# Performance work log

Measured on AMD Instinct MI355X. Metric: run time of the kernel, lower is better.

## Reference

```python
import jax, jax.numpy as jnp
import numpy as np
import math

HIDDEN = 768
HEADS = 12
HEAD_DIM = HIDDEN // HEADS
BLOCK = 256
TOPK = 3
BATCH = 2
SEQ = 2048


def setup_inputs() -> dict:
    key = jax.random.key(0)
    ks = jax.random.split(key, 5)
    s = 1.0 / math.sqrt(HIDDEN)
    return {
        "hidden_states": jax.random.normal(ks[0], (BATCH, SEQ, HIDDEN), jnp.float32),
        "Wq": jax.random.normal(ks[1], (HIDDEN, HIDDEN), jnp.float32) * s,
        "Wk": jax.random.normal(ks[2], (HIDDEN, HIDDEN), jnp.float32) * s,
        "Wv": jax.random.normal(ks[3], (HIDDEN, HIDDEN), jnp.float32) * s,
        "Wo": jax.random.normal(ks[4], (HIDDEN, HIDDEN), jnp.float32) * s,
    }


def _rope(x, sin, cos):
    # x: [B, H, S, D]; rotate-half RoPE
    d2 = x.shape[-1] // 2
    x1, x2 = x[..., :d2], x[..., d2:]
    return x * cos + jnp.concatenate([-x2, x1], axis=-1) * sin


def reference(hidden_states, Wq, Wk, Wv, Wo):
    B, S, Hd = hidden_states.shape
    H, D, bs, K = HEADS, HEAD_DIM, BLOCK, TOPK
    nb = S // bs  # number of key blocks
    scale = 1.0 / math.sqrt(D)

    def split_heads(x):
        return x.reshape(B, S, H, D).transpose(0, 2, 1, 3)  # [B,H,S,D]

    q = split_heads(hidden_states @ Wq.T)
    k = split_heads(hidden_states @ Wk.T)
    v = split_heads(hidden_states @ Wv.T)

    # rotary embedding (standard rotate-half RoPE, base 10000)
    inv_freq = 1.0 / (10000.0 ** (jnp.arange(0, D, 2, dtype=jnp.float32) / D))
    ang = jnp.arange(S, dtype=jnp.float32)[:, None] * inv_freq[None, :]  # [S, D/2]
    emb = jnp.concatenate([ang, ang], axis=-1)  # [S, D]
    sin, cos = jnp.sin(emb), jnp.cos(emb)
    q = _rope(q, sin, cos)
    k = _rope(k, sin, cos)

    # mean-pooled block representations of keys: [B,H,nb,D]
    block_reps = k.reshape(B, H, nb, bs, D).mean(axis=3)

    # routing scores: per-token score against each block rep
    bscores = jnp.einsum('bhsd,bhnd->bhsn', q, block_reps) * scale  # [B,H,S,nb]
    pos = jnp.arange(S)
    cur = pos // bs                       # current block of each query, [S]
    blk = jnp.arange(nb)
    future = blk[None, None, None, :] > cur[None, None, :, None]
    bscores = jnp.where(future, -jnp.inf, bscores)
    # current block is force-selected (score set to dtype max)
    is_cur = blk[None, None, None, :] == cur[None, None, :, None]
    bscores = jnp.where(is_cur, jnp.finfo(bscores.dtype).max, bscores)

    _, topk_idx = jax.lax.top_k(bscores, min(K, nb))  # [B,H,S,K]
    selected = jnp.sum(jax.nn.one_hot(topk_idx, nb, dtype=jnp.float32), axis=-2) > 0  # [B,H,S,nb]

    # per-key-position mask: key t allowed iff its block is selected for query i,
    # and within the current block only t <= i (matches original truncation).
    sel_t = selected[:, :, :, cur]                          # [B,H,Sq,Sk]
    intra_ok = (cur[None, :] != cur[:, None]) | (pos[None, :] <= pos[:, None])  # [Sq,Sk]
    mask = sel_t & intra_ok[None, None]

    scores = jnp.einsum('bhqd,bhkd->bhqk', q, k) * scale
    scores = jnp.where(mask, scores, -jnp.inf)
    probs = jax.nn.softmax(scores, axis=-1)
    out = jnp.einsum('bhqk,bhkd->bhqd', probs, v)

    out = out.transpose(0, 2, 1, 3).reshape(B, S, Hd)
    return out @ Wo.T
```

## Files before the change

### kernel.cpp

```cpp
#include <hip/hip_runtime.h>
#include <math.h>


#define HID   768
#define NH    12
#define DH    64
#define SEQN  2048
#define BATCH 2
#define NTOK  (BATCH*SEQN)
#define NB    8
#define BLKSZ 256
#define NEG_INF (-__builtin_huge_valf())
#define POS_INF (__builtin_huge_valf())
#define LO_SCALE 2048.0f
#define LO_INV   (1.0f/2048.0f)
#define EXP2C    0.18033688f

#define SPLIT_ROWS 1024
#define NBH   (BATCH*NH)

typedef unsigned short u16;
typedef _Float16 v8hf __attribute__((ext_vector_type(8)));
typedef float    v4f  __attribute__((ext_vector_type(4)));

__device__ __forceinline__ u16 f2h(float x) {
    _Float16 h = (_Float16)x;
    return __builtin_bit_cast(u16, h);
}
__device__ __forceinline__ float h2f(u16 u) {
    return (float)__builtin_bit_cast(_Float16, u);
}
__device__ __forceinline__ v8hf ldhf8(const u16* p) {
    return *reinterpret_cast<const v8hf*>(p);
}
__device__ __forceinline__ void g2lds16(const u16* g, u16* l) {
    __builtin_amdgcn_global_load_lds(
        (const __attribute__((address_space(1))) void*)g,
        (__attribute__((address_space(3))) void*)l, 16, 0, 0);
}
#define MFMA16(a, b, c) __builtin_amdgcn_mfma_f32_16x16x32_f16(a, b, c, 0, 0, 0)

__global__ __launch_bounds__(256)
void preproc_k(const float* __restrict__ X,  const float* __restrict__ Wq,
               const float* __restrict__ Wk, const float* __restrict__ Wv,
               const float* __restrict__ Wo, float2* __restrict__ tab,
               u16* __restrict__ Xh, u16* __restrict__ Xl,
               u16* __restrict__ Wq2, u16* __restrict__ Wk2,
               u16* __restrict__ Wv2, u16* __restrict__ Wo2)
{
    const int NW = HID * HID;
    const int id = blockIdx.x;
    const int tid = threadIdx.x;
    if (id < 12288) {
        const int i = id * 256 + tid;
        const float x = X[i];
        const u16 h = f2h(x);
        Xh[i] = h;
        Xl[i] = f2h((x - h2f(h)) * LO_SCALE);
    } else if (id < 21504) {
        const int j = (id - 12288) * 256 + tid;
        const int z = j / NW, i = j - z * NW;
        const float* src = (z == 0) ? Wq : (z == 1) ? Wk : (z == 2) ? Wv : Wo;
        u16* dst = (z == 0) ? Wq2 : (z == 1) ? Wk2 : (z == 2) ? Wv2 : Wo2;
        const float x = src[i];
        const u16 h = f2h(x);
        dst[i] = h;
        dst[i + NW] = f2h((x - h2f(h)) * LO_SCALE);
    } else {
        const int i = (id - 21504) * 256 + tid;
        const int s = i >> 5, f = i & 31;
        const double y  = exp((double)f * (log(10000.0) / 32.0));
        const float yf = (float)y;
        const float invf = 1.0f / yf;
        const float ang  = (float)s * invf;
        tab[i] = make_float2((float)sin((double)ang), (float)cos((double)ang));
    }
}

__device__ __forceinline__
void qkv_mainloop(const u16* __restrict__ Ah, const u16* __restrict__ Al,
                  const u16* __restrict__ Bh, const u16* __restrict__ Bl,
                  int m0, int nb0, int c_start,
                  u16* As, u16* Bs, v4f acc[2][4])
{
    const int tid = threadIdx.x;
    const int w = tid >> 6, lane = tid & 63;
    const int col = lane & 15, quad = lane >> 4;

    int a_row[4], a_gl[4];
    #pragma unroll
    for (int r = 0; r < 4; r++) {
        const int g = r * 256 + tid;
        a_row[r] = g >> 3;
        a_gl[r]  = (g & 7) ^ (a_row[r] & 7);
    }
    int b_row[2], b_gl[2];
    #pragma unroll
    for (int r = 0; r < 2; r++) {
        const int g = r * 256 + tid;
        b_row[r] = g >> 3;
        b_gl[r]  = (g & 7) ^ (b_row[r] & 7);
    }

    for (int c = c_start; c < 3; c++) {
        const u16* Ap = (c == 0) ? Al : Ah;
        const u16* Bp = (c == 1) ? Bl : Bh;
        for (int itc = 0; itc < HID / 64; itc++) {
            const int k0 = itc * 64;
            __syncthreads();
            #pragma unroll
            for (int r = 0; r < 4; r++)
                g2lds16(Ap + (size_t)(m0 + a_row[r]) * HID + k0 + a_gl[r] * 8,
                        &As[(r * 256 + w * 64) * 8]);
            #pragma unroll
            for (int r = 0; r < 2; r++)
                g2lds16(Bp + (size_t)(nb0 + b_row[r]) * HID + k0 + b_gl[r] * 8,
                        &Bs[(r * 256 + w * 64) * 8]);
            __syncthreads();
            #pragma unroll
            for (int ks = 0; ks < 2; ks++) {
                v8hf af[2], bf_[4];
                #pragma unroll
                for (int mt = 0; mt < 2; mt++) {
                    const int row = w * 32 + mt * 16 + col;
                    const int gph = (ks * 4 + quad) ^ (row & 7);
                    af[mt] = ldhf8(&As[row * 64 + gph * 8]);
                }
                #pragma unroll
                for (int nt = 0; nt < 4; nt++) {
                    const int row = nt * 16 + col;
                    const int gph = (ks * 4 + quad) ^ (row & 7);
                    bf_[nt] = ldhf8(&Bs[row * 64 + gph * 8]);
                }
                #pragma unroll
                for (int mt = 0; mt < 2; mt++)
                    #pragma unroll
                    for (int nt = 0; nt < 4; nt++)
                        acc[mt][nt] = MFMA16(af[mt], bf_[nt], acc[mt][nt]);
            }
        }
        if (c == 1) {
            #pragma unroll
            for (int mt = 0; mt < 2; mt++)
                #pragma unroll
                for (int nt = 0; nt < 4; nt++)
                    #pragma unroll
                    for (int r = 0; r < 4; r++)
                        acc[mt][nt][r] *= LO_INV;
        }
    }
    __syncthreads();
}

__global__ __launch_bounds__(256)
void qkv_fused_gemm_k(const u16* __restrict__ Xh, const u16* __restrict__ Xl,
                      const u16* __restrict__ Wq2, const u16* __restrict__ Wk2,
                      const u16* __restrict__ Wv2, const float2* __restrict__ tab,
                      float* __restrict__ q32, u16* __restrict__ kh16,
                      u16* __restrict__ vth, float* __restrict__ partial)
{
    __shared__ u16 As[128 * 64];
    __shared__ u16 Bs[64 * 64];
    __shared__ float psum[4][64];

    const int NW = HID * HID;
    const int id    = blockIdx.x;
    const int xcd   = id & 7, loc = id >> 3;
    const int mtile = xcd * 4 + (loc & 3);
    const int ntile = loc >> 2;
    const int m0  = mtile * 128;
    const int mat = ntile / 12;
    const int nb0 = (ntile - mat * 12) * 64;
    const u16* Bh = (mat == 0) ? Wq2 : (mat == 1) ? Wk2 : Wv2;

    v4f acc[2][4] = {};
    qkv_mainloop(Xh, Xl, Bh, Bh + NW, m0, nb0, (mat == 2) ? 1 : 0, As, Bs, acc);

    const int tid = threadIdx.x;
    const int w = tid >> 6, lane = tid & 63;
    const int col = lane & 15, quad = lane >> 4;
    const int b = m0 >> 11;
    const int h = nb0 >> 6;
    const size_t bh = (size_t)b * NH + h;

    if (mat == 2) {
        #pragma unroll
        for (int nt = 0; nt < 4; nt++) {
            const int d = nt * 16 + col;
            #pragma unroll
            for (int mt = 0; mt < 2; mt++) {
                const int m = m0 + w * 32 + mt * 16 + quad * 4;
                const int s = m & (SEQN - 1);
                ushort4 pk = make_ushort4(f2h(acc[mt][nt][0]), f2h(acc[mt][nt][1]),
                                          f2h(acc[mt][nt][2]), f2h(acc[mt][nt][3]));
                *(ushort4*)&vth[(bh * DH + d) * SEQN + s] = pk;
            }
        }
        return;
    }

    float vsum[4] = {0.f, 0.f, 0.f, 0.f};
    #pragma unroll
    for (int mt = 0; mt < 2; mt++) {
        #pragma unroll
        for (int nt = 0; nt < 4; nt++) {
            const int d = nt * 16 + col;
            #pragma unroll
            for (int r = 0; r < 4; r++) {
                const int m = m0 + w * 32 + mt * 16 + quad * 4 + r;
                const int s = m & (SEQN - 1);
                const float part = acc[mt][nt ^ 2][r];
                const float2 sc = tab[(s << 5) + (d & 31)];
                const float val = (d < 32) ? acc[mt][nt][r] * sc.y - part * sc.x
                                           : acc[mt][nt][r] * sc.y + part * sc.x;
                const size_t idx = (bh * SEQN + s) * DH + d;
                if (mat == 0) {
                    q32[idx] = val;
                } else {
                    kh16[idx] = f2h(val);
                    vsum[nt] += val;
                }
            }
        }
    }
    if (mat == 1) {
        #pragma unroll
        for (int nt = 0; nt < 4; nt++) {
            float v = vsum[nt];
            v += __shfl_xor(v, 16);
            v += __shfl_xor(v, 32);
            if (quad == 0) psum[w][nt * 16 + col] = v;
        }
        __syncthreads();
        if (tid < 64) {
            const float s4 = (psum[0][tid] + psum[1][tid])
                           + (psum[2][tid] + psum[3][tid]);
            const int nblk = (m0 & (SEQN - 1)) >> 8;
            const int half = (m0 >> 7) & 1;
            partial[((bh * NB + nblk) * 2 + half) * 64 + tid] = s4;
        }
    }
}

__global__ __launch_bounds__(256)
void out_gemm_mfma_k(const u16* __restrict__ Ah, const u16* __restrict__ Wo2,
                     float* __restrict__ C)
{
    __shared__ u16 As[64 * 64];
    __shared__ u16 Bs[64 * 64];

    const int NW = HID * HID;
    const int id    = blockIdx.x;
    const int xcd   = id & 7, loc = id >> 3;
    const int mtile = xcd * 8 + (loc & 7);
    const int ntile = loc >> 3;
    const int m0 = mtile * 64, n0 = ntile * 64;
    const int tid = threadIdx.x;
    const int w = tid >> 6, lane = tid & 63;
    const int col = lane & 15, quad = lane >> 4;

    const int r0 = tid >> 3,         gl0 = (tid & 7) ^ (r0 & 7);
    const int r1 = (256 + tid) >> 3, gl1 = ((256 + tid) & 7) ^ (r1 & 7);

    v4f acc[4] = {};
    #pragma unroll
    for (int c = 0; c < 2; c++) {
        const u16* Bp = (c == 0) ? (Wo2 + NW) : Wo2;
        for (int itc = 0; itc < HID / 64; itc++) {
            const int k0 = itc * 64;
            __syncthreads();
            g2lds16(Ah + (size_t)(m0 + r0) * HID + k0 + gl0 * 8, &As[(w * 64) * 8]);
            g2lds16(Ah + (size_t)(m0 + r1) * HID + k0 + gl1 * 8, &As[(256 + w * 64) * 8]);
            g2lds16(Bp + (size_t)(n0 + r0) * HID + k0 + gl0 * 8, &Bs[(w * 64) * 8]);
            g2lds16(Bp + (size_t)(n0 + r1) * HID + k0 + gl1 * 8, &Bs[(256 + w * 64) * 8]);
            __syncthreads();
            #pragma unroll
            for (int ks = 0; ks < 2; ks++) {
                const int arow = w * 16 + col;
                v8hf a = ldhf8(&As[arow * 64 + (((ks * 4 + quad) ^ (arow & 7))) * 8]);
                #pragma unroll
                for (int nt = 0; nt < 4; nt++) {
                    const int row = nt * 16 + col;
                    v8hf bb = ldhf8(&Bs[row * 64 + (((ks * 4 + quad) ^ (row & 7))) * 8]);
                    acc[nt] = MFMA16(a, bb, acc[nt]);
                }
            }
        }
        if (c == 0) {
            #pragma unroll
            for (int nt = 0; nt < 4; nt++)
                #pragma unroll
                for (int r = 0; r < 4; r++)
                    acc[nt][r] *= LO_INV;
        }
    }

    #pragma unroll
    for (int nt = 0; nt < 4; nt++)
        #pragma unroll
        for (int r = 0; r < 4; r++) {
            const int m = m0 + w * 16 + quad * 4 + r;
            C[(size_t)m * HID + n0 + nt * 16 + col] = acc[nt][r];
        }
}

__global__ __launch_bounds__(64)
void reps_reduce_k(const float* __restrict__ partial, float* __restrict__ reps)
{
    const int bhn = blockIdx.x;
    const int d = threadIdx.x;
    const float* p = &partial[(size_t)bhn * 128 + d];
    double s = (double)p[0] + (double)p[64];
    reps[(size_t)bhn * 64 + d] = (float)(s * (1.0 / 256.0));
}

__global__ __launch_bounds__(128)
void select_topk_k(const float* __restrict__ qg, const float* __restrict__ reps,
                   unsigned* __restrict__ selm)
{
    __shared__ float rs[NB][DH];
    const int bh = blockIdx.y;
    const int tid = threadIdx.x;
    for (int idx = tid; idx < NB * DH; idx += 128)
        rs[idx >> 6][idx & 63] = reps[(size_t)bh * NB * DH + idx];
    __syncthreads();

    const int qq = blockIdx.x * 128 + tid;
    const float* qv = &qg[((size_t)bh * SEQN + qq) * DH];
    float qr[DH];
    #pragma unroll
    for (int c = 0; c < 16; c++) {
        float4 t = *(const float4*)&qv[c * 4];
        qr[c*4+0]=t.x; qr[c*4+1]=t.y; qr[c*4+2]=t.z; qr[c*4+3]=t.w;
    }
    const int cur = qq >> 8;
    double sc[NB];
    #pragma unroll
    for (int n = 0; n < NB; n++) {
        double ssum = 0.0;
        for (int d = 0; d < DH; d++) ssum += (double)qr[d] * (double)rs[n][d];
        sc[n] = ssum * 0.125;
    }
    for (int n = cur + 1; n < NB; n++) sc[n] = -1e300;
    sc[cur] = 1e300;
    unsigned mask = 0;
    for (int p = 0; p < 3; p++) {
        int bi = -1; double bv = 0.0;
        for (int n = 0; n < NB; n++) {
            if ((mask >> n) & 1) continue;
            if (bi < 0 || sc[n] > bv) { bi = n; bv = sc[n]; }
        }
        mask |= 1u << bi;
    }
    selm[(size_t)bh * SEQN + qq] = mask;
}

__global__ __launch_bounds__(256, 5)
void moba_attn_k(const float* __restrict__ q32, const u16* __restrict__ kh16,
                 const u16* __restrict__ vth, const unsigned* __restrict__ selm,
                 u16* __restrict__ aoh, float* __restrict__ po,
                 float* __restrict__ ml)
{
    __shared__ u16 kbuf[2][64 * 64];
    __shared__ u16 vbuf[64 * 64];
    __shared__ u16 plds[4][16][64];
    unsigned* s_uni = (unsigned*)&plds[0][0][0];

    const int id  = blockIdx.x;
    const int xcd = id & 7, loc = id >> 3;
    const int bh  = xcd * 3 + loc / 48;
    const int u   = loc % 48;
    int qb, split, stride;
    if (u < 16) { qb = u;                 split = 0;          stride = 1; }
    else        { qb = 16 + ((u - 16) >> 1); split = (u - 16) & 1; stride = 2; }
    const int q0  = qb * 64;
    const int cur = q0 >> 8;
    const int tid = threadIdx.x;
    const int wave = tid >> 6, lane = tid & 63;
    const int col = lane & 15, quad = lane >> 4;
    const int qw0 = q0 + wave * 16;
    const int qpos = qw0 + col;
    const size_t bhS = (size_t)bh * SEQN;
    const size_t bhV = (size_t)bh * DH;

    if (tid == 0) *s_uni = 0;
    __syncthreads();
    const unsigned mymask = selm[bhS + qw0 + col];
    unsigned uw = mymask;
    #pragma unroll
    for (int off = 1; off < 16; off <<= 1) uw |= __shfl_xor(uw, off);
    if (lane == 0) atomicOr(s_uni, uw);
    const unsigned wmask = __builtin_amdgcn_readfirstlane(uw);

    v8hf qh[2], ql[2];
    #pragma unroll
    for (int ks = 0; ks < 2; ks++) {
        const float* qp = &q32[(bhS + qw0 + col) * DH + ks * 32 + quad * 8];
        float4 f0 = *(const float4*)qp;
        float4 f1 = *(const float4*)(qp + 4);
        float qf[8] = {f0.x, f0.y, f0.z, f0.w, f1.x, f1.y, f1.z, f1.w};
        union { u16 u[8]; v8hf h; } uh, ul;
        #pragma unroll
        for (int j = 0; j < 8; j++) {
            u16 hb = f2h(qf[j]);
            uh.u[j] = hb;
            ul.u[j] = f2h((qf[j] - h2f(hb)) * LO_SCALE);
        }
        qh[ks] = uh.h; ql[ks] = ul.h;
    }
    __syncthreads();
    const unsigned uni = __builtin_amdgcn_readfirstlane(*s_uni);

    int n_nxt = __builtin_ctz(uni), c_nxt = 0;
    bool has_nxt = true;
    auto c2max = [&](int n) { return (n == cur) ? ((q0 + 63 - n * BLKSZ) >> 6) : 3; };
    auto advance1 = [&]() {
        if (c_nxt < c2max(n_nxt)) { c_nxt++; return; }
        for (int nn = n_nxt + 1; nn < NB; nn++)
            if ((uni >> nn) & 1) { n_nxt = nn; c_nxt = 0; return; }
        has_nxt = false;
    };
    for (int i = 0; i < split; i++) if (has_nxt) advance1();
    int n_cur = n_nxt, c_cur = c_nxt;
    const bool cur_valid = has_nxt;

    const size_t srow0 = (size_t)bh * SPLIT_ROWS + (q0 - SPLIT_ROWS);

    if (!cur_valid) {
        if (stride == 2) {
            if (quad == 0) {
                const size_t r = srow0 + wave * 16 + col;
                ml[(r * 2 + split) * 2 + 0] = NEG_INF;
                ml[(r * 2 + split) * 2 + 1] = 0.f;
            }
            #pragma unroll
            for (int nt = 0; nt < 4; nt++)
                #pragma unroll
                for (int r = 0; r < 4; r++) {
                    const size_t rq = srow0 + wave * 16 + quad * 4 + r;
                    po[(rq * 2 + split) * 64 + nt * 16 + col] = 0.f;
                }
        }
        return;
    }
    for (int i = 0; i < stride; i++) if (has_nxt) advance1();

    const int sg_row0 = tid >> 3;
    const int sg_gl0  = (tid & 7) ^ (sg_row0 & 7);
    const int sg_row1 = (256 + tid) >> 3;
    const int sg_gl1  = ((256 + tid) & 7) ^ (sg_row1 & 7);
    auto stage_k = [&](int n, int c2, int buf) {
        const int kb = n * BLKSZ + c2 * 64;
        u16* kd = (u16*)kbuf[buf];
        g2lds16(kh16 + (bhS + kb + sg_row0) * DH + sg_gl0 * 8, kd + (wave * 64) * 8);
        g2lds16(kh16 + (bhS + kb + sg_row1) * DH + sg_gl1 * 8, kd + (256 + wave * 64) * 8);
    };
    auto stage_v = [&](int n, int c2) {
        const int kb = n * BLKSZ + c2 * 64;
        u16* vd = (u16*)vbuf;
        g2lds16(vth + (bhV + sg_row0) * SEQN + kb + sg_gl0 * 8, vd + (wave * 64) * 8);
        g2lds16(vth + (bhV + sg_row1) * SEQN + kb + sg_gl1 * 8, vd + (256 + wave * 64) * 8);
    };

    const v4f zero4 = {0.f, 0.f, 0.f, 0.f};
    v4f oacc[4] = {zero4, zero4, zero4, zero4};
    float m_i = NEG_INF, l_i = 0.f;
    const int psw = (col & 7) << 1;

    stage_k(n_cur, c_cur, 0);
    int t = 0;
    while (true) {
        asm volatile("s_waitcnt lgkmcnt(0)" ::: "memory");
        __builtin_amdgcn_s_barrier();
        __builtin_amdgcn_sched_barrier(0);

        stage_v(n_cur, c_cur);
        if (has_nxt) stage_k(n_nxt, c_nxt, (t + 1) & 1);
        else         stage_k(n_cur, c_cur, (t + 1) & 1);

        asm volatile("s_waitcnt vmcnt(4)" ::: "memory");
        __builtin_amdgcn_sched_barrier(0);

        const int n  = n_cur;
        const bool act = (wmask >> n) & 1;
        if (act) {
            const int kb = n * BLKSZ + c_cur * 64;
            const bool iscur = (n == cur);
            const float selinf = ((mymask >> n) & 1) ? 0.f : POS_INF;
            const bool need_mask = iscur && (kb + 63 > qw0);
            const u16* kd = (const u16*)kbuf[t & 1];

            v4f sf[4];
            __builtin_amdgcn_s_setprio(1);
            #pragma unroll
            for (int mt = 0; mt < 4; mt++) {
                const int row = mt * 16 + col;
                const int r7 = row & 7;
                v8hf kh0 = ldhf8(&kd[(row * 8 + (quad ^ r7)) * 8]);
                v8hf kh1 = ldhf8(&kd[(row * 8 + ((4 + quad) ^ r7)) * 8]);
                v4f c = zero4;
                c = MFMA16(kh0, ql[0], c);
                c = MFMA16(kh1, ql[1], c);
                #pragma unroll
                for (int r = 0; r < 4; r++) c[r] *= LO_INV;
                c = MFMA16(kh0, qh[0], c);
                c = MFMA16(kh1, qh[1], c);
                sf[mt] = c;
            }
            __builtin_amdgcn_s_setprio(0);

            if (need_mask) {
                #pragma unroll
                for (int mt = 0; mt < 4; mt++)
                    #pragma unroll
                    for (int r = 0; r < 4; r++) {
                        const int kidx = kb + mt * 16 + quad * 4 + r;
                        sf[mt][r] = (kidx <= qpos) ? sf[mt][r] : NEG_INF;
                    }
            }

            float rm = NEG_INF;
            #pragma unroll
            for (int mt = 0; mt < 4; mt++)
                #pragma unroll
                for (int r = 0; r < 4; r++) rm = fmaxf(rm, sf[mt][r]);
            rm = fmaxf(rm, __shfl_xor(rm, 16));
            rm = fmaxf(rm, __shfl_xor(rm, 32));
            rm = rm - selinf;
            const float mnew  = fmaxf(m_i, rm);
            const float alpha = (m_i == NEG_INF) ? 0.f : exp2f((m_i - mnew) * EXP2C);
            const float biasC = ((mnew == NEG_INF) ? 0.f : mnew * EXP2C) + selinf;

            float lsum = 0.f;
            #pragma unroll
            for (int mt = 0; mt < 4; mt++) {
                ushort4 hv;
                #pragma unroll
                for (int r = 0; r < 4; r++) {
                    float p = exp2f(fmaf(sf[mt][r], EXP2C, -biasC));
                    lsum += p;
                    u16 hu = f2h(p);
                    if (r == 0) hv.x = hu;
                    else if (r == 1) hv.y = hu;
                    else if (r == 2) hv.z = hu;
                    else hv.w = hu;
                }
                *(ushort4*)&plds[wave][col][((mt * 4 + quad) ^ psw) * 4] = hv;
            }
            lsum += __shfl_xor(lsum, 16);
            lsum += __shfl_xor(lsum, 32);
            l_i = l_i * alpha + lsum;
            m_i = mnew;

            float ar[4];
            #pragma unroll
            for (int r = 0; r < 4; r++) ar[r] = __shfl(alpha, quad * 4 + r, 16);
            #pragma unroll
            for (int nt = 0; nt < 4; nt++)
                #pragma unroll
                for (int r = 0; r < 4; r++) oacc[nt][r] *= ar[r];

            __threadfence_block();
        }

        asm volatile("s_waitcnt vmcnt(2)" ::: "memory");
        __builtin_amdgcn_sched_barrier(0);

        if (act) {
            const u16* vd = (const u16*)vbuf;
            __builtin_amdgcn_s_setprio(1);
            #pragma unroll
            for (int ks2 = 0; ks2 < 2; ks2++) {
                v8hf ph = ldhf8(&plds[wave][col][((ks2 * 8 + quad * 2) ^ psw) * 4]);
                #pragma unroll
                for (int nt = 0; nt < 4; nt++) {
                    const int row = nt * 16 + col;
                    const int g = (ks2 * 4 + quad) ^ (row & 7);
                    v8hf vh = ldhf8(&vd[(row * 8 + g) * 8]);
                    oacc[nt] = MFMA16(ph, vh, oacc[nt]);
                }
            }
            __builtin_amdgcn_s_setprio(0);
        }

        if (!has_nxt) break;
        n_cur = n_nxt; c_cur = c_nxt;
        for (int i = 0; i < stride; i++) if (has_nxt) advance1();
        t++;
    }

    if (stride == 2) {
        if (quad == 0) {
            const size_t r = srow0 + wave * 16 + col;
            ml[(r * 2 + split) * 2 + 0] = m_i;
            ml[(r * 2 + split) * 2 + 1] = l_i;
        }
        #pragma unroll
        for (int nt = 0; nt < 4; nt++)
            #pragma unroll
            for (int r = 0; r < 4; r++) {
                const size_t rq = srow0 + wave * 16 + quad * 4 + r;
                po[(rq * 2 + split) * 64 + nt * 16 + col] = oacc[nt][r];
            }
        return;
    }

    const int b = bh / NH, h = bh % NH;
    const float invl = 1.f / l_i;
    float ir[4];
    #pragma unroll
    for (int r = 0; r < 4; r++) ir[r] = __shfl(invl, quad * 4 + r, 16);
    #pragma unroll
    for (int nt = 0; nt < 4; nt++)
        #pragma unroll
        for (int r = 0; r < 4; r++) {
            const int qi = qw0 + quad * 4 + r;
            const size_t idx = ((size_t)b * SEQN + qi) * HID + h * DH + nt * 16 + col;
            aoh[idx] = f2h(oacc[nt][r] * ir[r]);
        }
}

__global__ __launch_bounds__(256)
void attn_combine_k(const float* __restrict__ po, const float* __restrict__ ml,
                    u16* __restrict__ aoh)
{
    const int g = blockIdx.x * 256 + threadIdx.x;
    const int d = g & 63;
    const size_t row = (size_t)(g >> 6);
    const int bh = (int)(row >> 10);
    const int qlocal = (int)(row & 1023);
    const float m0 = ml[(row * 2 + 0) * 2 + 0], l0 = ml[(row * 2 + 0) * 2 + 1];
    const float m1 = ml[(row * 2 + 1) * 2 + 0], l1 = ml[(row * 2 + 1) * 2 + 1];
    const float m  = fmaxf(m0, m1);
    const float a0 = (m0 == NEG_INF) ? 0.f : exp2f((m0 - m) * EXP2C);
    const float a1 = (m1 == NEG_INF) ? 0.f : exp2f((m1 - m) * EXP2C);
    const float o  = po[(row * 2 + 0) * 64 + d] * a0
                   + po[(row * 2 + 1) * 64 + d] * a1;
    const float inv = 1.f / (l0 * a0 + l1 * a1);
    const int b = bh / NH, h = bh % NH;
    const int q = SPLIT_ROWS + qlocal;
    aoh[((size_t)b * SEQN + q) * HID + h * DH + d] = f2h(o * inv);
}

extern "C" void kernel_launch(void* const* d_in, const int* in_sizes, int n_in,
                              void* d_out, int out_size, void* d_ws, size_t ws_size,
                              hipStream_t stream)
{
    const float* X  = (const float*)d_in[0];
    const float* Wq = (const float*)d_in[1];
    const float* Wk = (const float*)d_in[2];
    const float* Wv = (const float*)d_in[3];
    const float* Wo = (const float*)d_in[4];
    float* out = (float*)d_out;

    char* p = (char*)d_ws;
    float* q32 = (float*)p;                p += (size_t)NTOK*HID*4;
    u16* kh16 = (u16*)p;                   p += (size_t)NTOK*HID*2;
    u16* vth  = (u16*)p;                   p += (size_t)NTOK*HID*2;
    u16* Xh   = (u16*)p;                   p += (size_t)NTOK*HID*2;
    u16* Xl   = (u16*)p;                   p += (size_t)NTOK*HID*2;
    u16* Wq2  = (u16*)p;                   p += (size_t)HID*HID*2*2;
    u16* Wk2  = (u16*)p;                   p += (size_t)HID*HID*2*2;
    u16* Wv2  = (u16*)p;                   p += (size_t)HID*HID*2*2;
    u16* Wo2  = (u16*)p;                   p += (size_t)HID*HID*2*2;
    float* partial = (float*)p;            p += (size_t)BATCH*NH*NB*2*64*4;
    float* reps    = (float*)p;            p += (size_t)BATCH*NH*NB*DH*4;
    unsigned* selm = (unsigned*)p;         p += (size_t)BATCH*NH*SEQN*4;
    float2* tab    = (float2*)p;           p += (size_t)SEQN*32*8;
    u16* aoh = Xh;

    float* po = (float*)Xl;
    float* ml = po + (size_t)NBH * SPLIT_ROWS * 2 * 64;

    preproc_k<<<dim3(21760), 256, 0, stream>>>(X, Wq, Wk, Wv, Wo, tab,
                                               Xh, Xl, Wq2, Wk2, Wv2, Wo2);

    qkv_fused_gemm_k<<<dim3(1152), 256, 0, stream>>>(
        Xh, Xl, Wq2, Wk2, Wv2, tab, q32, kh16, vth, partial);

    reps_reduce_k<<<dim3(BATCH*NH*NB), 64, 0, stream>>>(partial, reps);
    select_topk_k<<<dim3(SEQN/128, BATCH*NH), 128, 0, stream>>>(q32, reps, selm);

    moba_attn_k<<<dim3(1152), 256, 0, stream>>>(
        q32, kh16, vth, selm, aoh, po, ml);

    attn_combine_k<<<dim3(6144), 256, 0, stream>>>(po, ml, aoh);

    out_gemm_mfma_k<<<dim3(768), 256, 0, stream>>>(aoh, Wo2, out);
}
```

Before: 241.8 us.

## Load V tiles directly from global into registers instead of staging through LDS

Removes the shared-memory V buffer and its async global-to-LDS staging. Each wave now loads its V operand fragments straight from global memory into registers after the QK MFMAs and feeds them to the PV MFMAs. The explicit vmcnt/lgkmcnt pipelining is replaced with a plain __syncthreads. This cuts LDS usage and the LDS round trip, but each of the four waves now fetches the whole V tile, which multiplies V global/L2 traffic. It also loses the overlap of the V load with the QK compute and may raise register pressure.

```diff
diff --git a/kernel.cpp b/kernel.cpp
--- a/kernel.cpp
+++ b/kernel.cpp
@@ -362,7 +362,6 @@
                  float* __restrict__ ml)
 {
     __shared__ u16 kbuf[2][64 * 64];
-    __shared__ u16 vbuf[64 * 64];
     __shared__ u16 plds[4][16][64];
     unsigned* s_uni = (unsigned*)&plds[0][0][0];
 
@@ -455,12 +454,6 @@
         g2lds16(kh16 + (bhS + kb + sg_row0) * DH + sg_gl0 * 8, kd + (wave * 64) * 8);
         g2lds16(kh16 + (bhS + kb + sg_row1) * DH + sg_gl1 * 8, kd + (256 + wave * 64) * 8);
     };
-    auto stage_v = [&](int n, int c2) {
-        const int kb = n * BLKSZ + c2 * 64;
-        u16* vd = (u16*)vbuf;
-        g2lds16(vth + (bhV + sg_row0) * SEQN + kb + sg_gl0 * 8, vd + (wave * 64) * 8);
-        g2lds16(vth + (bhV + sg_row1) * SEQN + kb + sg_gl1 * 8, vd + (256 + wave * 64) * 8);
-    };
 
     const v4f zero4 = {0.f, 0.f, 0.f, 0.f};
     v4f oacc[4] = {zero4, zero4, zero4, zero4};
@@ -470,20 +463,11 @@
     stage_k(n_cur, c_cur, 0);
     int t = 0;
     while (true) {
-        asm volatile("s_waitcnt lgkmcnt(0)" ::: "memory");
-        __builtin_amdgcn_s_barrier();
-        __builtin_amdgcn_sched_barrier(0);
-
-        stage_v(n_cur, c_cur);
+        __syncthreads();
         if (has_nxt) stage_k(n_nxt, c_nxt, (t + 1) & 1);
-        else         stage_k(n_cur, c_cur, (t + 1) & 1);
-
-        asm volatile("s_waitcnt vmcnt(4)" ::: "memory");
-        __builtin_amdgcn_sched_barrier(0);
 
         const int n  = n_cur;
-        const bool act = (wmask >> n) & 1;
-        if (act) {
+        if ((wmask >> n) & 1) {
             const int kb = n * BLKSZ + c_cur * 64;
             const bool iscur = (n == cur);
             const float selinf = ((mymask >> n) & 1) ? 0.f : POS_INF;
@@ -508,6 +492,15 @@
                 sf[mt] = c;
             }
             __builtin_amdgcn_s_setprio(0);
+
+            v8hf vg0[4], vg1[4];
+            #pragma unroll
+            for (int nt = 0; nt < 4; nt++) {
+                const int row = nt * 16 + col;
+                const u16* vp = vth + (bhV + row) * SEQN + kb + quad * 8;
+                vg0[nt] = ldhf8(vp);
+                vg1[nt] = ldhf8(vp + 32);
+            }
 
             if (need_mask) {
                 #pragma unroll
@@ -561,24 +554,14 @@
                 for (int r = 0; r < 4; r++) oacc[nt][r] *= ar[r];
 
             __threadfence_block();
-        }
-
-        asm volatile("s_waitcnt vmcnt(2)" ::: "memory");
-        __builtin_amdgcn_sched_barrier(0);
-
-        if (act) {
-            const u16* vd = (const u16*)vbuf;
+
             __builtin_amdgcn_s_setprio(1);
             #pragma unroll
             for (int ks2 = 0; ks2 < 2; ks2++) {
                 v8hf ph = ldhf8(&plds[wave][col][((ks2 * 8 + quad * 2) ^ psw) * 4]);
                 #pragma unroll
-                for (int nt = 0; nt < 4; nt++) {
-                    const int row = nt * 16 + col;
-                    const int g = (ks2 * 4 + quad) ^ (row & 7);
-                    v8hf vh = ldhf8(&vd[(row * 8 + g) * 8]);
-                    oacc[nt] = MFMA16(ph, vh, oacc[nt]);
-                }
+                for (int nt = 0; nt < 4; nt++)
+                    oacc[nt] = MFMA16(ph, (ks2 == 0) ? vg0[nt] : vg1[nt], oacc[nt]);
             }
             __builtin_amdgcn_s_setprio(0);
         }
```

Measured after the change: 327.1 us. 1.35x slower.
